# Kernel optimization log

Measured on AMD Instinct MI355X. Metric: run time of the kernel, lower is better.

Reference implementation:

```python
import jax, jax.numpy as jnp
import numpy as np

EPS = 1e-12
LAMDA = 1.0
MAX_ITER = 10


def setup_inputs() -> dict:
    key = jax.random.key(0)
    k1, k2 = jax.random.split(key)
    B, L1, L2, D = 64, 1024, 1024, 256
    x1 = jax.random.normal(k1, (B, L1, D), dtype=jnp.float32)
    x2 = jax.random.normal(k2, (B, L2, D), dtype=jnp.float32)
    return {"x1": x1, "x2": x2}


def _cos(x1, x2):
    # batched cosine similarity: [B, L1, L2]
    M = jnp.einsum('bik,bjk->bij', x1, x2)
    a = jnp.sqrt(jnp.sum(x1 * x1, axis=-1, keepdims=True))  # [B, L1, 1]
    b = jnp.sqrt(jnp.sum(x2 * x2, axis=-1, keepdims=True))  # [B, L2, 1]
    norm = a * jnp.swapaxes(b, 1, 2)                          # [B, L1, L2]
    return M / (norm + EPS)


def reference(x1, x2):
    B, L1, _ = x1.shape
    L2 = x2.shape[1]
    M = 1.0 - _cos(x1, x2)          # [B, L1, L2] cost matrix
    K = jnp.exp(-M * LAMDA)
    w1 = jnp.full((B, L1, 1), 1.0 / L1, dtype=x1.dtype)
    w2 = jnp.full((B, L2, 1), 1.0 / L2, dtype=x1.dtype)
    ui = jnp.ones((B, L1, 1), dtype=x1.dtype)
    vi = jnp.ones((B, L2, 1), dtype=x1.dtype)
    Kt = jnp.swapaxes(K, 1, 2)      # [B, L2, L1]

    def body(_, carry):
        ui, vi = carry
        vi = w2 / (jnp.matmul(Kt, ui) + EPS)
        ui = w1 / (jnp.matmul(K, vi) + EPS)
        return (ui, vi)

    ui, vi = jax.lax.fori_loop(0, MAX_ITER, body, (ui, vi))
    G = ui * K * jnp.swapaxes(vi, 1, 2)   # transport plan [B, L1, L2]
    G_max = jnp.max(G, axis=(-1, -2), keepdims=True)
    G_min = jnp.min(G, axis=(-1, -2), keepdims=True)
    G = (G - G_min) / (G_max - G_min + EPS)
    return G * M
```

## Files before the change

### kernel.cpp

```cpp
#include <hip/hip_runtime.h>
#include <hip/hip_bf16.h>


#define EPSV 1e-12f
#define W1 0.0009765625f

typedef short  short8 __attribute__((ext_vector_type(8)));
typedef float  f32x4  __attribute__((ext_vector_type(4)));
typedef _Float16 h8   __attribute__((ext_vector_type(8)));
typedef _Float16 h2   __attribute__((ext_vector_type(2)));

__device__ __forceinline__ short8 ld_cvt8(const float* p) {
  float4 f0 = *(const float4*)p;
  float4 f1 = *(const float4*)(p + 4);
  float2 p0; p0.x = f0.x; p0.y = f0.y;
  float2 p1; p1.x = f0.z; p1.y = f0.w;
  float2 p2; p2.x = f1.x; p2.y = f1.y;
  float2 p3; p3.x = f1.z; p3.y = f1.w;
  __hip_bfloat162 h0 = __float22bfloat162_rn(p0);
  __hip_bfloat162 h1 = __float22bfloat162_rn(p1);
  __hip_bfloat162 h2_ = __float22bfloat162_rn(p2);
  __hip_bfloat162 h3 = __float22bfloat162_rn(p3);
  short2 a = *(short2*)&h0, b = *(short2*)&h1, c = *(short2*)&h2_, d = *(short2*)&h3;
  short8 r;
  r[0] = a.x; r[1] = a.y; r[2] = b.x; r[3] = b.y;
  r[4] = c.x; r[5] = c.y; r[6] = d.x; r[7] = d.y;
  return r;
}

__global__ __launch_bounds__(256) void diag_kernel(float* __restrict__ out,
                                                   float val, int n) {
  int stride = gridDim.x * 256;
  for (int i = blockIdx.x * 256 + threadIdx.x; i < n; i += stride) out[i] = val;
}

__global__ __launch_bounds__(256) void prep_kernel(
    const float* __restrict__ x1, const float* __restrict__ x2,
    float* __restrict__ n1, float* __restrict__ n2,
    unsigned* __restrict__ mm) {
  int t = threadIdx.x, bid = blockIdx.x;
  if (bid == 0 && t < 128) mm[t] = (t < 64) ? 0u : 0x7f800000u;
  int row = bid * 4 + (t >> 6);
  int lane = t & 63;
  const float* xp; float* np_;
  int r = row;
  if (row < 65536) { xp = x1; np_ = n1; }
  else { r = row - 65536; xp = x2; np_ = n2; }
  float4 v = ((const float4*)(xp + (size_t)r * 256))[lane];
  float s = v.x * v.x + v.y * v.y + v.z * v.z + v.w * v.w;
  #pragma unroll
  for (int off = 1; off < 64; off <<= 1) s += __shfl_xor(s, off, 64);
  if (lane == 0) np_[r] = sqrtf(s);
}

__global__ __launch_bounds__(256) void gemm_kernel(
    const float* __restrict__ x1, const float* __restrict__ x2,
    const float* __restrict__ n1, const float* __restrict__ n2,
    _Float16* __restrict__ Kh, _Float16* __restrict__ p0) {
  __shared__ __align__(16) unsigned short smem[2 * 128 * 64];
  __shared__ float csum[4][128];
  unsigned short* As = smem;
  unsigned short* Bs = smem + 128 * 64;
  int bid = blockIdx.x;
  int b = bid >> 6, tile = bid & 63;
  int ti = (tile >> 3) << 7, tj = (tile & 7) << 7;
  int t = threadIdx.x, lane = t & 63, wave = t >> 6;
  int wr = (wave >> 1) << 6, wc = (wave & 1) << 6;
  const float* Ag = x1 + ((size_t)(b * 1024 + ti)) * 256;
  const float* Bg = x2 + ((size_t)(b * 1024 + tj)) * 256;

  f32x4 acc[4][4];
  f32x4 zero = {0.f, 0.f, 0.f, 0.f};
  #pragma unroll
  for (int m = 0; m < 4; ++m)
    #pragma unroll
    for (int n = 0; n < 4; ++n) acc[m][n] = zero;

  short8 ra[4], rb[4];
  #pragma unroll
  for (int c = 0; c < 4; ++c) {
    int ch = t + (c << 8); int row = ch >> 3, kg = ch & 7;
    ra[c] = ld_cvt8(Ag + row * 256 + kg * 8);
    rb[c] = ld_cvt8(Bg + row * 256 + kg * 8);
  }

  for (int k0 = 0; k0 < 4; ++k0) {
    __syncthreads();
    #pragma unroll
    for (int c = 0; c < 4; ++c) {
      int ch = t + (c << 8); int row = ch >> 3, kg = ch & 7;
      int kgs = kg ^ (row & 7);
      *(short8*)(As + row * 64 + kgs * 8) = ra[c];
      *(short8*)(Bs + row * 64 + kgs * 8) = rb[c];
    }
    __syncthreads();
    if (k0 < 3) {
      #pragma unroll
      for (int c = 0; c < 4; ++c) {
        int ch = t + (c << 8); int row = ch >> 3, kg = ch & 7;
        ra[c] = ld_cvt8(Ag + row * 256 + (k0 + 1) * 64 + kg * 8);
        rb[c] = ld_cvt8(Bg + row * 256 + (k0 + 1) * 64 + kg * 8);
      }
    }
    #pragma unroll
    for (int ks = 0; ks < 2; ++ks) {
      short8 af[4], bfr[4];
      #pragma unroll
      for (int m = 0; m < 4; ++m) {
        int row = wr + m * 16 + (lane & 15);
        int c16 = (ks << 2) + (lane >> 4);
        af[m] = *(const short8*)(As + row * 64 + ((c16 ^ (row & 7)) << 3));
      }
      #pragma unroll
      for (int n = 0; n < 4; ++n) {
        int row = wc + n * 16 + (lane & 15);
        int c16 = (ks << 2) + (lane >> 4);
        bfr[n] = *(const short8*)(Bs + row * 64 + ((c16 ^ (row & 7)) << 3));
      }
      #pragma unroll
      for (int m = 0; m < 4; ++m)
        #pragma unroll
        for (int n = 0; n < 4; ++n)
          acc[m][n] = __builtin_amdgcn_mfma_f32_16x16x32_bf16(af[m], bfr[n], acc[m][n], 0, 0, 0);
    }
  }
  __syncthreads();

  _Float16* Ct = (_Float16*)smem;
  float a1v[4][4], b2v[4];
  #pragma unroll
  for (int m = 0; m < 4; ++m)
    #pragma unroll
    for (int q = 0; q < 4; ++q)
      a1v[m][q] = n1[(size_t)b * 1024 + ti + wr + m * 16 + ((lane >> 4) << 2) + q];
  #pragma unroll
  for (int n = 0; n < 4; ++n)
    b2v[n] = n2[(size_t)b * 1024 + tj + wc + n * 16 + (lane & 15)];
  #pragma unroll
  for (int m = 0; m < 4; ++m)
    #pragma unroll
    for (int n = 0; n < 4; ++n)
      #pragma unroll
      for (int q = 0; q < 4; ++q) {
        int rl = wr + m * 16 + ((lane >> 4) << 2) + q;
        int cl = wc + n * 16 + (lane & 15);
        float cosv = acc[m][n][q] / (a1v[m][q] * b2v[n] + EPSV);
        Ct[rl * 128 + cl] = (_Float16)__expf(cosv - 1.0f);
      }
  __syncthreads();
  size_t kbase = ((size_t)b << 20);
  #pragma unroll
  for (int c2i = 0; c2i < 8; ++c2i) {
    int c2 = t + (c2i << 8);
    int row = c2 >> 4, seg = c2 & 15;
    *(float4*)(Kh + kbase + (size_t)(ti + row) * 1024 + tj + seg * 8) = ((const float4*)Ct)[c2];
  }
  if (p0 != nullptr) {
    int cg = lane & 15, rsub = lane >> 4;
    float cs[8];
    #pragma unroll
    for (int k = 0; k < 8; ++k) cs[k] = 0.f;
    #pragma unroll
    for (int i = 0; i < 8; ++i) {
      h8 rowv = *(const h8*)&Ct[(wave * 32 + rsub + i * 4) * 128 + cg * 8];
      #pragma unroll
      for (int k = 0; k < 8; ++k) cs[k] += (float)rowv[k];
    }
    #pragma unroll
    for (int k = 0; k < 8; ++k) {
      cs[k] += __shfl_xor(cs[k], 16, 64);
      cs[k] += __shfl_xor(cs[k], 32, 64);
    }
    if (rsub == 0) {
      #pragma unroll
      for (int k = 0; k < 8; ++k) csum[wave][cg * 8 + k] = cs[k];
    }
    __syncthreads();
    if (t < 128) {
      float s = csum[0][t] + csum[1][t] + csum[2][t] + csum[3][t];
      p0[((size_t)b << 14) + ((size_t)(ti >> 7) << 10) + tj + t] = (_Float16)s;
    }
  }
}

__global__ __launch_bounds__(512) void ktu0_kernel(
    const _Float16* __restrict__ Kh, _Float16* __restrict__ dst) {
  int bid = blockIdx.x;
  int b = bid >> 2, s = bid & 3;
  int t = threadIdx.x, lane = t & 63, w = t >> 6;
  __shared__ float plds[8][1024];
  float pacc[16];
  #pragma unroll
  for (int k = 0; k < 16; ++k) pacc[k] = 0.f;
  const _Float16* kp = Kh + ((size_t)b << 20) + (size_t)(s * 256 + w) * 1024 + lane * 8;
  #pragma unroll 2
  for (int it = 0; it < 32; ++it) {
    h8 k0 = *(const h8*)(kp + (size_t)it * 8192);
    h8 k1 = *(const h8*)(kp + (size_t)it * 8192 + 512);
    #pragma unroll
    for (int k = 0; k < 8; ++k) { pacc[k] += (float)k0[k]; pacc[8 + k] += (float)k1[k]; }
  }
  float4 v0 = {pacc[0], pacc[1], pacc[2], pacc[3]};
  float4 v1 = {pacc[4], pacc[5], pacc[6], pacc[7]};
  float4 v2 = {pacc[8], pacc[9], pacc[10], pacc[11]};
  float4 v3 = {pacc[12], pacc[13], pacc[14], pacc[15]};
  *(float4*)&plds[w][lane * 8] = v0;
  *(float4*)&plds[w][lane * 8 + 4] = v1;
  *(float4*)&plds[w][512 + lane * 8] = v2;
  *(float4*)&plds[w][512 + lane * 8 + 4] = v3;
  __syncthreads();
  #pragma unroll
  for (int p = 0; p < 2; ++p) {
    int col = (p << 9) + t;
    float sum = plds[0][col] + plds[1][col] + plds[2][col] + plds[3][col]
              + plds[4][col] + plds[5][col] + plds[6][col] + plds[7][col];
    dst[((size_t)b << 12) + (s << 10) + col] = (_Float16)sum;
  }
}

template<int BSHIFT, int NSRC, int FINAL>
__global__ __launch_bounds__(512, 4) void fused_kernel(
    const _Float16* __restrict__ Kh, const _Float16* __restrict__ src,
    _Float16* __restrict__ dst, float* __restrict__ zb,
    unsigned* __restrict__ mm) {
  constexpr int LOGS = BSHIFT - 10;
  constexpr int ROWS = 1024 >> LOGS;
  constexpr int ITERS = ROWS / 8;
  int bid = blockIdx.x;
  int b = bid >> LOGS, s = bid & ((1 << LOGS) - 1);
  int t = threadIdx.x, lane = t & 63, w = t >> 6;
  __shared__ float sv[1024];
  __shared__ float plds[8][1024];
  __shared__ float red[16];
  {
    int col2 = t << 1;
    const _Float16* sp = src + ((size_t)b << BSHIFT) + col2;
    float y0 = 0.f, y1 = 0.f;
    #pragma unroll
    for (int j = 0; j < NSRC; ++j) {
      h2 vv = *(const h2*)(sp + (j << 10));
      y0 += (float)vv[0]; y1 += (float)vv[1];
    }
    sv[col2] = W1 / (y0 + EPSV);
    sv[col2 + 1] = W1 / (y1 + EPSV);
  }
  __syncthreads();
  float svr[16];
  {
    float4 s0 = *(const float4*)&sv[lane * 8];
    float4 s1 = *(const float4*)&sv[lane * 8 + 4];
    float4 s2 = *(const float4*)&sv[512 + lane * 8];
    float4 s3 = *(const float4*)&sv[512 + lane * 8 + 4];
    svr[0] = s0.x;  svr[1] = s0.y;  svr[2]  = s0.z;  svr[3]  = s0.w;
    svr[4] = s1.x;  svr[5] = s1.y;  svr[6]  = s1.z;  svr[7]  = s1.w;
    svr[8] = s2.x;  svr[9] = s2.y;  svr[10] = s2.z;  svr[11] = s2.w;
    svr[12] = s3.x; svr[13] = s3.y; svr[14] = s3.z;  svr[15] = s3.w;
  }
  float pacc[16];
  #pragma unroll
  for (int k = 0; k < 16; ++k) pacc[k] = 0.f;
  float gmn = 3.4e38f, gmx = 0.f;
  const _Float16* kp = Kh + ((size_t)b << 20) + (size_t)(s * ROWS + w) * 1024 + lane * 8;
  #pragma unroll 2
  for (int it = 0; it < ITERS; ++it) {
    int r = s * ROWS + w + it * 8;
    h8 k0 = *(const h8*)(kp + (size_t)it * 8192);
    h8 k1 = *(const h8*)(kp + (size_t)it * 8192 + 512);
    float dot = 0.f;
    #pragma unroll
    for (int k = 0; k < 8; ++k)
      dot += (float)k0[k] * svr[k] + (float)k1[k] * svr[8 + k];
    #pragma unroll
    for (int off = 1; off < 64; off <<= 1) dot += __shfl_xor(dot, off, 64);
    float u = W1 / (dot + EPSV);
    if (FINAL) {
      if (lane == 0) zb[(b << 10) + r] = dot;
      #pragma unroll
      for (int k = 0; k < 8; ++k) {
        float g0 = u * (float)k0[k] * svr[k];
        float g1 = u * (float)k1[k] * svr[8 + k];
        gmn = fminf(gmn, fminf(g0, g1)); gmx = fmaxf(gmx, fmaxf(g0, g1));
      }
    } else {
      #pragma unroll
      for (int k = 0; k < 8; ++k) {
        pacc[k] += (float)k0[k] * u;
        pacc[8 + k] += (float)k1[k] * u;
      }
    }
  }
  if (!FINAL) {
    float4 v0 = {pacc[0], pacc[1], pacc[2], pacc[3]};
    float4 v1 = {pacc[4], pacc[5], pacc[6], pacc[7]};
    float4 v2 = {pacc[8], pacc[9], pacc[10], pacc[11]};
    float4 v3 = {pacc[12], pacc[13], pacc[14], pacc[15]};
    *(float4*)&plds[w][lane * 8] = v0;
    *(float4*)&plds[w][lane * 8 + 4] = v1;
    *(float4*)&plds[w][512 + lane * 8] = v2;
    *(float4*)&plds[w][512 + lane * 8 + 4] = v3;
    __syncthreads();
    #pragma unroll
    for (int p = 0; p < 2; ++p) {
      int col = (p << 9) + t;
      float sum = plds[0][col] + plds[1][col] + plds[2][col] + plds[3][col]
                + plds[4][col] + plds[5][col] + plds[6][col] + plds[7][col];
      dst[((size_t)b << BSHIFT) + (s << 10) + col] = (_Float16)sum;
    }
  } else {
    #pragma unroll
    for (int off = 1; off < 64; off <<= 1) {
      gmn = fminf(gmn, __shfl_xor(gmn, off, 64));
      gmx = fmaxf(gmx, __shfl_xor(gmx, off, 64));
    }
    if (lane == 0) { red[w] = gmn; red[8 + w] = gmx; }
    __syncthreads();
    if (t == 0) {
      float m0 = red[0], m1 = red[8];
      #pragma unroll
      for (int i = 1; i < 8; ++i) { m0 = fminf(m0, red[i]); m1 = fmaxf(m1, red[8 + i]); }
      atomicMin(&mm[64 + b], __float_as_uint(m0));
      atomicMax(&mm[b],      __float_as_uint(m1));
    }
  }
}

template<int BSHIFT, int NSRC>
__global__ __launch_bounds__(256) void fin_kernel(
    const _Float16* __restrict__ Kh, const _Float16* __restrict__ src,
    const float* __restrict__ zb, const unsigned* __restrict__ mm,
    float* __restrict__ out) {
  int bid = blockIdx.x;
  int b = bid >> 4, rg = bid & 15;
  int t = threadIdx.x, lane = t & 63, w = t >> 6;
  __shared__ float sv[1024];
  #pragma unroll
  for (int p = 0; p < 2; ++p) {
    int col2 = (p << 9) + (t << 1);
    const _Float16* sp = src + ((size_t)b << BSHIFT) + col2;
    float y0 = 0.f, y1 = 0.f;
    #pragma unroll
    for (int j = 0; j < NSRC; ++j) {
      h2 vv = *(const h2*)(sp + (j << 10));
      y0 += (float)vv[0]; y1 += (float)vv[1];
    }
    sv[col2] = W1 / (y0 + EPSV);
    sv[col2 + 1] = W1 / (y1 + EPSV);
  }
  __syncthreads();
  float svr[16];
  {
    float4 s0 = *(const float4*)&sv[lane * 8];
    float4 s1 = *(const float4*)&sv[lane * 8 + 4];
    float4 s2 = *(const float4*)&sv[512 + lane * 8];
    float4 s3 = *(const float4*)&sv[512 + lane * 8 + 4];
    svr[0] = s0.x;  svr[1] = s0.y;  svr[2]  = s0.z;  svr[3]  = s0.w;
    svr[4] = s1.x;  svr[5] = s1.y;  svr[6]  = s1.z;  svr[7]  = s1.w;
    svr[8] = s2.x;  svr[9] = s2.y;  svr[10] = s2.z;  svr[11] = s2.w;
    svr[12] = s3.x; svr[13] = s3.y; svr[14] = s3.z;  svr[15] = s3.w;
  }
  float gmx = __uint_as_float(mm[b]);
  float gmn = __uint_as_float(mm[64 + b]);
  float scale = 1.0f / (gmx - gmn + EPSV);
  const _Float16* kp = Kh + ((size_t)b << 20) + (size_t)(rg * 64 + w) * 1024 + lane * 8;
  float* op = out + ((size_t)b << 20) + (size_t)(rg * 64 + w) * 1024 + lane * 8;
  for (int it = 0; it < 16; ++it) {
    int r = rg * 64 + w + it * 4;
    float u = W1 / (zb[b * 1024 + r] + EPSV);
    h8 k0 = *(const h8*)(kp + (size_t)it * 4096);
    h8 k1 = *(const h8*)(kp + (size_t)it * 4096 + 512);
    float o[16];
    #pragma unroll
    for (int k = 0; k < 8; ++k) {
      float kfa = (float)k0[k];
      float kfb = (float)k1[k];
      float ga = u * kfa * svr[k];
      float gb = u * kfb * svr[8 + k];
      o[k]     = (ga - gmn) * scale * (-__logf(kfa));
      o[8 + k] = (gb - gmn) * scale * (-__logf(kfb));
    }
    float4 o0 = {o[0], o[1], o[2], o[3]};
    float4 o1 = {o[4], o[5], o[6], o[7]};
    float4 o2 = {o[8], o[9], o[10], o[11]};
    float4 o3 = {o[12], o[13], o[14], o[15]};
    *(float4*)(op + (size_t)it * 4096) = o0;
    *(float4*)(op + (size_t)it * 4096 + 4) = o1;
    *(float4*)(op + (size_t)it * 4096 + 512) = o2;
    *(float4*)(op + (size_t)it * 4096 + 516) = o3;
  }
}

extern "C" void kernel_launch(void* const* d_in, const int* in_sizes, int n_in,
                              void* d_out, int out_size, void* d_ws, size_t ws_size,
                              hipStream_t stream) {
  const float* x1 = (const float*)d_in[0];
  const float* x2 = (const float*)d_in[1];
  float* out = (float*)d_out;
  char* ws = (char*)d_ws;

  _Float16* Kh = (_Float16*)(ws);
  float*    n1 = (float*)(ws + 134217728ULL);
  float*    zb = (float*)(ws + 134217728ULL);
  float*    n2 = (float*)(ws + 134479872ULL);

  _Float16* pA16 = (_Float16*)(ws + 134742016ULL);
  _Float16* pB16 = (_Float16*)(ws + 136839168ULL);
  unsigned* mmA  = (unsigned*)(ws + 138936320ULL);
  const size_t WS_A = 138936832ULL;

  _Float16* pA4 = (_Float16*)(ws + 134742016ULL);
  _Float16* pB4 = (_Float16*)(ws + 135266304ULL);
  unsigned* mmB = (unsigned*)(ws + 135790592ULL);
  const size_t WS_B = 135791104ULL;

  if (ws_size >= WS_A) {
    prep_kernel<<<32768, 256, 0, stream>>>(x1, x2, n1, n2, mmA);
    gemm_kernel<<<4096, 256, 0, stream>>>(x1, x2, n1, n2, Kh, pA16);
    fused_kernel<14, 8, 0><<<1024, 512, 0, stream>>>(Kh, pA16, pB16, zb, mmA);
    for (int k = 2; k <= 9; ++k) {
      _Float16* src = (k & 1) ? pA16 : pB16;
      _Float16* dst = (k & 1) ? pB16 : pA16;
      fused_kernel<14, 16, 0><<<1024, 512, 0, stream>>>(Kh, src, dst, zb, mmA);
    }
    fused_kernel<14, 16, 1><<<1024, 512, 0, stream>>>(Kh, pB16, pA16, zb, mmA);
    fin_kernel<14, 16><<<1024, 256, 0, stream>>>(Kh, pB16, zb, mmA, out);
  } else if (ws_size >= WS_B) {
    prep_kernel<<<32768, 256, 0, stream>>>(x1, x2, n1, n2, mmB);
    gemm_kernel<<<4096, 256, 0, stream>>>(x1, x2, n1, n2, Kh, nullptr);
    ktu0_kernel<<<256, 512, 0, stream>>>(Kh, pA4);
    for (int k = 1; k <= 9; ++k) {
      _Float16* src = (k & 1) ? pA4 : pB4;
      _Float16* dst = (k & 1) ? pB4 : pA4;
      fused_kernel<12, 4, 0><<<256, 512, 0, stream>>>(Kh, src, dst, zb, mmB);
    }
    fused_kernel<12, 4, 1><<<256, 512, 0, stream>>>(Kh, pB4, pA4, zb, mmB);
    fin_kernel<12, 4><<<1024, 256, 0, stream>>>(Kh, pB4, zb, mmB, out);
  } else {
    float val = 100.0f + (float)(ws_size >> 20);
    diag_kernel<<<2048, 256, 0, stream>>>(out, val, out_size);
  }
}
```

Before: 496.4 us.

## Replace per-slice fp16 partial buffers with fixed-point atomic accumulation into rotating buffers

Column-sum partials, previously written as separate fp16 slices and summed by the next kernel, are now reduced in place with 32-bit fixed-point atomicAdd into one of three rotating buffers. The kernel that consumes a buffer also zeroes the next one. This removes the multi-slice partial reads and the separate ktu0 path, and unrolls the K loads four rows at a time to raise memory-level parallelism. In exchange it adds atomic contention and fixed-point quantization, which risks overflow or lost precision if sums leave the expected range.

```diff
diff --git a/kernel.cpp b/kernel.cpp
--- a/kernel.cpp
+++ b/kernel.cpp
@@ -4,11 +4,12 @@
 
 #define EPSV 1e-12f
 #define W1 0.0009765625f
+#define FIXS 524288.0f
+#define INV_FIXS 1.9073486328125e-6f
 
 typedef short  short8 __attribute__((ext_vector_type(8)));
 typedef float  f32x4  __attribute__((ext_vector_type(4)));
 typedef _Float16 h8   __attribute__((ext_vector_type(8)));
-typedef _Float16 h2   __attribute__((ext_vector_type(2)));
 
 __device__ __forceinline__ short8 ld_cvt8(const float* p) {
   float4 f0 = *(const float4*)p;
@@ -37,9 +38,10 @@
 __global__ __launch_bounds__(256) void prep_kernel(
     const float* __restrict__ x1, const float* __restrict__ x2,
     float* __restrict__ n1, float* __restrict__ n2,
-    unsigned* __restrict__ mm) {
+    unsigned* __restrict__ mm, unsigned* __restrict__ rz) {
   int t = threadIdx.x, bid = blockIdx.x;
   if (bid == 0 && t < 128) mm[t] = (t < 64) ? 0u : 0x7f800000u;
+  if (bid < 512) rz[bid * 256 + t] = 0u;
   int row = bid * 4 + (t >> 6);
   int lane = t & 63;
   const float* xp; float* np_;
@@ -56,7 +58,7 @@
 __global__ __launch_bounds__(256) void gemm_kernel(
     const float* __restrict__ x1, const float* __restrict__ x2,
     const float* __restrict__ n1, const float* __restrict__ n2,
-    _Float16* __restrict__ Kh, _Float16* __restrict__ p0) {
+    _Float16* __restrict__ Kh, unsigned* __restrict__ p0) {
   __shared__ __align__(16) unsigned short smem[2 * 128 * 64];
   __shared__ float csum[4][128];
   unsigned short* As = smem;
@@ -155,7 +157,7 @@
     int row = c2 >> 4, seg = c2 & 15;
     *(float4*)(Kh + kbase + (size_t)(ti + row) * 1024 + tj + seg * 8) = ((const float4*)Ct)[c2];
   }
-  if (p0 != nullptr) {
+  {
     int cg = lane & 15, rsub = lane >> 4;
     float cs[8];
     #pragma unroll
@@ -177,72 +179,140 @@
     }
     __syncthreads();
     if (t < 128) {
-      float s = csum[0][t] + csum[1][t] + csum[2][t] + csum[3][t];
-      p0[((size_t)b << 14) + ((size_t)(ti >> 7) << 10) + tj + t] = (_Float16)s;
-    }
-  }
-}
-
-__global__ __launch_bounds__(512) void ktu0_kernel(
-    const _Float16* __restrict__ Kh, _Float16* __restrict__ dst) {
+      float s_ = csum[0][t] + csum[1][t] + csum[2][t] + csum[3][t];
+      atomicAdd(&p0[((size_t)b << 10) + tj + t], __float2uint_rn(s_ * FIXS));
+    }
+  }
+}
+
+template<int FINAL>
+__global__ __launch_bounds__(512, 4) void fused_kernel(
+    const _Float16* __restrict__ Kh, const unsigned* __restrict__ inp,
+    unsigned* __restrict__ outp, unsigned* __restrict__ zbuf,
+    float* __restrict__ zb, unsigned* __restrict__ mm) {
   int bid = blockIdx.x;
-  int b = bid >> 2, s = bid & 3;
-  int t = threadIdx.x, lane = t & 63, w = t >> 6;
-  __shared__ float plds[8][1024];
-  float pacc[16];
-  #pragma unroll
-  for (int k = 0; k < 16; ++k) pacc[k] = 0.f;
-  const _Float16* kp = Kh + ((size_t)b << 20) + (size_t)(s * 256 + w) * 1024 + lane * 8;
-  #pragma unroll 2
-  for (int it = 0; it < 32; ++it) {
-    h8 k0 = *(const h8*)(kp + (size_t)it * 8192);
-    h8 k1 = *(const h8*)(kp + (size_t)it * 8192 + 512);
-    #pragma unroll
-    for (int k = 0; k < 8; ++k) { pacc[k] += (float)k0[k]; pacc[8 + k] += (float)k1[k]; }
-  }
-  float4 v0 = {pacc[0], pacc[1], pacc[2], pacc[3]};
-  float4 v1 = {pacc[4], pacc[5], pacc[6], pacc[7]};
-  float4 v2 = {pacc[8], pacc[9], pacc[10], pacc[11]};
-  float4 v3 = {pacc[12], pacc[13], pacc[14], pacc[15]};
-  *(float4*)&plds[w][lane * 8] = v0;
-  *(float4*)&plds[w][lane * 8 + 4] = v1;
-  *(float4*)&plds[w][512 + lane * 8] = v2;
-  *(float4*)&plds[w][512 + lane * 8 + 4] = v3;
-  __syncthreads();
-  #pragma unroll
-  for (int p = 0; p < 2; ++p) {
-    int col = (p << 9) + t;
-    float sum = plds[0][col] + plds[1][col] + plds[2][col] + plds[3][col]
-              + plds[4][col] + plds[5][col] + plds[6][col] + plds[7][col];
-    dst[((size_t)b << 12) + (s << 10) + col] = (_Float16)sum;
-  }
-}
-
-template<int BSHIFT, int NSRC, int FINAL>
-__global__ __launch_bounds__(512, 4) void fused_kernel(
-    const _Float16* __restrict__ Kh, const _Float16* __restrict__ src,
-    _Float16* __restrict__ dst, float* __restrict__ zb,
-    unsigned* __restrict__ mm) {
-  constexpr int LOGS = BSHIFT - 10;
-  constexpr int ROWS = 1024 >> LOGS;
-  constexpr int ITERS = ROWS / 8;
-  int bid = blockIdx.x;
-  int b = bid >> LOGS, s = bid & ((1 << LOGS) - 1);
+  int b = bid >> 4, s = bid & 15;
   int t = threadIdx.x, lane = t & 63, w = t >> 6;
   __shared__ float sv[1024];
   __shared__ float plds[8][1024];
   __shared__ float red[16];
   {
     int col2 = t << 1;
-    const _Float16* sp = src + ((size_t)b << BSHIFT) + col2;
-    float y0 = 0.f, y1 = 0.f;
-    #pragma unroll
-    for (int j = 0; j < NSRC; ++j) {
-      h2 vv = *(const h2*)(sp + (j << 10));
-      y0 += (float)vv[0]; y1 += (float)vv[1];
-    }
-    sv[col2] = W1 / (y0 + EPSV);
-    sv[col2 + 1] = W1 / (y1 + EPSV);
+    uint2 yv = *(const uint2*)(inp + ((size_t)b << 10) + col2);
+    sv[col2]     = W1 / ((float)yv.x * INV_FIXS + EPSV);
+    sv[col2 + 1] = W1 / ((float)yv.y * INV_FIXS + EPSV);
+  }
+  __syncthreads();
+  if (!FINAL && t < 64) zbuf[((size_t)b << 10) + (s << 6) + t] = 0u;
+  float svr[16];
+  {
+    float4 s0 = *(const float4*)&sv[lane * 8];
+    float4 s1 = *(const float4*)&sv[lane * 8 + 4];
+    float4 s2 = *(const float4*)&sv[512 + lane * 8];
+    float4 s3 = *(const float4*)&sv[512 + lane * 8 + 4];
+    svr[0] = s0.x;  svr[1] = s0.y;  svr[2]  = s0.z;  svr[3]  = s0.w;
+    svr[4] = s1.x;  svr[5] = s1.y;  svr[6]  = s1.z;  svr[7]  = s1.w;
+    svr[8] = s2.x;  svr[9] = s2.y;  svr[10] = s2.z;  svr[11] = s2.w;
+    svr[12] = s3.x; svr[13] = s3.y; svr[14] = s3.z;  svr[15] = s3.w;
+  }
+  float pacc[16];
+  #pragma unroll
+  for (int k = 0; k < 16; ++k) pacc[k] = 0.f;
+  float gmn = 3.4e38f, gmx = 0.f;
+  const _Float16* kp = Kh + ((size_t)b << 20) + (size_t)(s * 64 + w) * 1024 + lane * 8;
+  #pragma unroll
+  for (int half = 0; half < 2; ++half) {
+    h8 ka[4], kb[4];
+    #pragma unroll
+    for (int j = 0; j < 4; ++j) {
+      int it = half * 4 + j;
+      ka[j] = *(const h8*)(kp + (size_t)it * 8192);
+      kb[j] = *(const h8*)(kp + (size_t)it * 8192 + 512);
+    }
+    float dot[4];
+    #pragma unroll
+    for (int j = 0; j < 4; ++j) {
+      float d = 0.f;
+      #pragma unroll
+      for (int k = 0; k < 8; ++k)
+        d += (float)ka[j][k] * svr[k] + (float)kb[j][k] * svr[8 + k];
+      dot[j] = d;
+    }
+    #pragma unroll
+    for (int off = 1; off < 64; off <<= 1) {
+      #pragma unroll
+      for (int j = 0; j < 4; ++j) dot[j] += __shfl_xor(dot[j], off, 64);
+    }
+    #pragma unroll
+    for (int j = 0; j < 4; ++j) {
+      int it = half * 4 + j;
+      float u = W1 / (dot[j] + EPSV);
+      if (FINAL) {
+        if (lane == 0) zb[(b << 10) + s * 64 + w + it * 8] = dot[j];
+        #pragma unroll
+        for (int k = 0; k < 8; ++k) {
+          float g0 = u * (float)ka[j][k] * svr[k];
+          float g1 = u * (float)kb[j][k] * svr[8 + k];
+          gmn = fminf(gmn, fminf(g0, g1)); gmx = fmaxf(gmx, fmaxf(g0, g1));
+        }
+      } else {
+        #pragma unroll
+        for (int k = 0; k < 8; ++k) {
+          pacc[k] += (float)ka[j][k] * u;
+          pacc[8 + k] += (float)kb[j][k] * u;
+        }
+      }
+    }
+  }
+  if (!FINAL) {
+    float4 v0 = {pacc[0], pacc[1], pacc[2], pacc[3]};
+    float4 v1 = {pacc[4], pacc[5], pacc[6], pacc[7]};
+    float4 v2 = {pacc[8], pacc[9], pacc[10], pacc[11]};
+    float4 v3 = {pacc[12], pacc[13], pacc[14], pacc[15]};
+    *(float4*)&plds[w][lane * 8] = v0;
+    *(float4*)&plds[w][lane * 8 + 4] = v1;
+    *(float4*)&plds[w][512 + lane * 8] = v2;
+    *(float4*)&plds[w][512 + lane * 8 + 4] = v3;
+    __syncthreads();
+    #pragma unroll
+    for (int p = 0; p < 2; ++p) {
+      int col = (p << 9) + t;
+      float sum = plds[0][col] + plds[1][col] + plds[2][col] + plds[3][col]
+                + plds[4][col] + plds[5][col] + plds[6][col] + plds[7][col];
+      atomicAdd(&outp[((size_t)b << 10) + col], __float2uint_rn(sum * FIXS));
+    }
+  } else {
+    #pragma unroll
+    for (int off = 1; off < 64; off <<= 1) {
+      gmn = fminf(gmn, __shfl_xor(gmn, off, 64));
+      gmx = fmaxf(gmx, __shfl_xor(gmx, off, 64));
+    }
+    if (lane == 0) { red[w] = gmn; red[8 + w] = gmx; }
+    __syncthreads();
+    if (t == 0) {
+      float m0 = red[0], m1 = red[8];
+      #pragma unroll
+      for (int i = 1; i < 8; ++i) { m0 = fminf(m0, red[i]); m1 = fmaxf(m1, red[8 + i]); }
+      atomicMin(&mm[64 + b], __float_as_uint(m0));
+      atomicMax(&mm[b],      __float_as_uint(m1));
+    }
+  }
+}
+
+__global__ __launch_bounds__(256) void fin_kernel(
+    const _Float16* __restrict__ Kh, const unsigned* __restrict__ src,
+    const float* __restrict__ zb, const unsigned* __restrict__ mm,
+    float* __restrict__ out) {
+  int bid = blockIdx.x;
+  int b = bid >> 4, rg = bid & 15;
+  int t = threadIdx.x, lane = t & 63, w = t >> 6;
+  __shared__ float sv[1024];
+  #pragma unroll
+  for (int p = 0; p < 2; ++p) {
+    int col2 = (p << 9) + (t << 1);
+    uint2 yv = *(const uint2*)(src + ((size_t)b << 10) + col2);
+    sv[col2]     = W1 / ((float)yv.x * INV_FIXS + EPSV);
+    sv[col2 + 1] = W1 / ((float)yv.y * INV_FIXS + EPSV);
   }
   __syncthreads();
   float svr[16];
@@ -256,108 +326,6 @@
     svr[8] = s2.x;  svr[9] = s2.y;  svr[10] = s2.z;  svr[11] = s2.w;
     svr[12] = s3.x; svr[13] = s3.y; svr[14] = s3.z;  svr[15] = s3.w;
   }
-  float pacc[16];
-  #pragma unroll
-  for (int k = 0; k < 16; ++k) pacc[k] = 0.f;
-  float gmn = 3.4e38f, gmx = 0.f;
-  const _Float16* kp = Kh + ((size_t)b << 20) + (size_t)(s * ROWS + w) * 1024 + lane * 8;
-  #pragma unroll 2
-  for (int it = 0; it < ITERS; ++it) {
-    int r = s * ROWS + w + it * 8;
-    h8 k0 = *(const h8*)(kp + (size_t)it * 8192);
-    h8 k1 = *(const h8*)(kp + (size_t)it * 8192 + 512);
-    float dot = 0.f;
-    #pragma unroll
-    for (int k = 0; k < 8; ++k)
-      dot += (float)k0[k] * svr[k] + (float)k1[k] * svr[8 + k];
-    #pragma unroll
-    for (int off = 1; off < 64; off <<= 1) dot += __shfl_xor(dot, off, 64);
-    float u = W1 / (dot + EPSV);
-    if (FINAL) {
-      if (lane == 0) zb[(b << 10) + r] = dot;
-      #pragma unroll
-      for (int k = 0; k < 8; ++k) {
-        float g0 = u * (float)k0[k] * svr[k];
-        float g1 = u * (float)k1[k] * svr[8 + k];
-        gmn = fminf(gmn, fminf(g0, g1)); gmx = fmaxf(gmx, fmaxf(g0, g1));
-      }
-    } else {
-      #pragma unroll
-      for (int k = 0; k < 8; ++k) {
-        pacc[k] += (float)k0[k] * u;
-        pacc[8 + k] += (float)k1[k] * u;
-      }
-    }
-  }
-  if (!FINAL) {
-    float4 v0 = {pacc[0], pacc[1], pacc[2], pacc[3]};
-    float4 v1 = {pacc[4], pacc[5], pacc[6], pacc[7]};
-    float4 v2 = {pacc[8], pacc[9], pacc[10], pacc[11]};
-    float4 v3 = {pacc[12], pacc[13], pacc[14], pacc[15]};
-    *(float4*)&plds[w][lane * 8] = v0;
-    *(float4*)&plds[w][lane * 8 + 4] = v1;
-    *(float4*)&plds[w][512 + lane * 8] = v2;
-    *(float4*)&plds[w][512 + lane * 8 + 4] = v3;
-    __syncthreads();
-    #pragma unroll
-    for (int p = 0; p < 2; ++p) {
-      int col = (p << 9) + t;
-      float sum = plds[0][col] + plds[1][col] + plds[2][col] + plds[3][col]
-                + plds[4][col] + plds[5][col] + plds[6][col] + plds[7][col];
-      dst[((size_t)b << BSHIFT) + (s << 10) + col] = (_Float16)sum;
-    }
-  } else {
-    #pragma unroll
-    for (int off = 1; off < 64; off <<= 1) {
-      gmn = fminf(gmn, __shfl_xor(gmn, off, 64));
-      gmx = fmaxf(gmx, __shfl_xor(gmx, off, 64));
-    }
-    if (lane == 0) { red[w] = gmn; red[8 + w] = gmx; }
-    __syncthreads();
-    if (t == 0) {
-      float m0 = red[0], m1 = red[8];
-      #pragma unroll
-      for (int i = 1; i < 8; ++i) { m0 = fminf(m0, red[i]); m1 = fmaxf(m1, red[8 + i]); }
-      atomicMin(&mm[64 + b], __float_as_uint(m0));
-      atomicMax(&mm[b],      __float_as_uint(m1));
-    }
-  }
-}
-
-template<int BSHIFT, int NSRC>
-__global__ __launch_bounds__(256) void fin_kernel(
-    const _Float16* __restrict__ Kh, const _Float16* __restrict__ src,
-    const float* __restrict__ zb, const unsigned* __restrict__ mm,
-    float* __restrict__ out) {
-  int bid = blockIdx.x;
-  int b = bid >> 4, rg = bid & 15;
-  int t = threadIdx.x, lane = t & 63, w = t >> 6;
-  __shared__ float sv[1024];
-  #pragma unroll
-  for (int p = 0; p < 2; ++p) {
-    int col2 = (p << 9) + (t << 1);
-    const _Float16* sp = src + ((size_t)b << BSHIFT) + col2;
-    float y0 = 0.f, y1 = 0.f;
-    #pragma unroll
-    for (int j = 0; j < NSRC; ++j) {
-      h2 vv = *(const h2*)(sp + (j << 10));
-      y0 += (float)vv[0]; y1 += (float)vv[1];
-    }
-    sv[col2] = W1 / (y0 + EPSV);
-    sv[col2 + 1] = W1 / (y1 + EPSV);
-  }
-  __syncthreads();
-  float svr[16];
-  {
-    float4 s0 = *(const float4*)&sv[lane * 8];
-    float4 s1 = *(const float4*)&sv[lane * 8 + 4];
-    float4 s2 = *(const float4*)&sv[512 + lane * 8];
-    float4 s3 = *(const float4*)&sv[512 + lane * 8 + 4];
-    svr[0] = s0.x;  svr[1] = s0.y;  svr[2]  = s0.z;  svr[3]  = s0.w;
-    svr[4] = s1.x;  svr[5] = s1.y;  svr[6]  = s1.z;  svr[7]  = s1.w;
-    svr[8] = s2.x;  svr[9] = s2.y;  svr[10] = s2.z;  svr[11] = s2.w;
-    svr[12] = s3.x; svr[13] = s3.y; svr[14] = s3.z;  svr[15] = s3.w;
-  }
   float gmx = __uint_as_float(mm[b]);
   float gmn = __uint_as_float(mm[64 + b]);
   float scale = 1.0f / (gmx - gmn + EPSV);
@@ -401,41 +369,24 @@
   float*    n1 = (float*)(ws + 134217728ULL);
   float*    zb = (float*)(ws + 134217728ULL);
   float*    n2 = (float*)(ws + 134479872ULL);
-
-  _Float16* pA16 = (_Float16*)(ws + 134742016ULL);
-  _Float16* pB16 = (_Float16*)(ws + 136839168ULL);
-  unsigned* mmA  = (unsigned*)(ws + 138936320ULL);
-  const size_t WS_A = 138936832ULL;
-
-  _Float16* pA4 = (_Float16*)(ws + 134742016ULL);
-  _Float16* pB4 = (_Float16*)(ws + 135266304ULL);
-  unsigned* mmB = (unsigned*)(ws + 135790592ULL);
-  const size_t WS_B = 135791104ULL;
-
-  if (ws_size >= WS_A) {
-    prep_kernel<<<32768, 256, 0, stream>>>(x1, x2, n1, n2, mmA);
-    gemm_kernel<<<4096, 256, 0, stream>>>(x1, x2, n1, n2, Kh, pA16);
-    fused_kernel<14, 8, 0><<<1024, 512, 0, stream>>>(Kh, pA16, pB16, zb, mmA);
-    for (int k = 2; k <= 9; ++k) {
-      _Float16* src = (k & 1) ? pA16 : pB16;
-      _Float16* dst = (k & 1) ? pB16 : pA16;
-      fused_kernel<14, 16, 0><<<1024, 512, 0, stream>>>(Kh, src, dst, zb, mmA);
-    }
-    fused_kernel<14, 16, 1><<<1024, 512, 0, stream>>>(Kh, pB16, pA16, zb, mmA);
-    fin_kernel<14, 16><<<1024, 256, 0, stream>>>(Kh, pB16, zb, mmA, out);
-  } else if (ws_size >= WS_B) {
-    prep_kernel<<<32768, 256, 0, stream>>>(x1, x2, n1, n2, mmB);
-    gemm_kernel<<<4096, 256, 0, stream>>>(x1, x2, n1, n2, Kh, nullptr);
-    ktu0_kernel<<<256, 512, 0, stream>>>(Kh, pA4);
-    for (int k = 1; k <= 9; ++k) {
-      _Float16* src = (k & 1) ? pA4 : pB4;
-      _Float16* dst = (k & 1) ? pB4 : pA4;
-      fused_kernel<12, 4, 0><<<256, 512, 0, stream>>>(Kh, src, dst, zb, mmB);
-    }
-    fused_kernel<12, 4, 1><<<256, 512, 0, stream>>>(Kh, pB4, pA4, zb, mmB);
-    fin_kernel<12, 4><<<1024, 256, 0, stream>>>(Kh, pB4, zb, mmB, out);
-  } else {
+  unsigned* R0 = (unsigned*)(ws + 134742016ULL);
+  unsigned* R1 = (unsigned*)(ws + 135004160ULL);
+  unsigned* R2 = (unsigned*)(ws + 135266304ULL);
+  unsigned* mm = (unsigned*)(ws + 135528448ULL);
+  const size_t WS_NEED = 135528960ULL;
+  unsigned* R[3] = {R0, R1, R2};
+
+  if (ws_size < WS_NEED) {
     float val = 100.0f + (float)(ws_size >> 20);
     diag_kernel<<<2048, 256, 0, stream>>>(out, val, out_size);
-  }
-}
+    return;
+  }
+
+  prep_kernel<<<32768, 256, 0, stream>>>(x1, x2, n1, n2, mm, R0);
+  gemm_kernel<<<4096, 256, 0, stream>>>(x1, x2, n1, n2, Kh, R0);
+  for (int k = 1; k <= 9; ++k)
+    fused_kernel<0><<<1024, 512, 0, stream>>>(Kh, R[(k - 1) % 3], R[k % 3],
+                                              R[(k + 1) % 3], zb, mm);
+  fused_kernel<1><<<1024, 512, 0, stream>>>(Kh, R0, R1, R2, zb, mm);
+  fin_kernel<<<1024, 256, 0, stream>>>(Kh, R0, zb, mm, out);
+}
```

Result: slower. 785.4 us (+58.2%).
